# Optimization experiments

Measured on AMD Instinct MI355X. Metric: run time of the kernel, lower is better.

Reference implementation:

```python
import jax, jax.numpy as jnp
import numpy as np

N_ATOMS = 200000
MAX_DEG = 6
DEG_COUNTS = [2000, 40000, 60000, 58000, 38000, 1500, 500]  # atoms of degree 0..6, sorted by degree
_OFF = np.concatenate([[0], np.cumsum(DEG_COUNTS)])
BATCH = 1024
N_TASKS = 12
NAF = 75
BN_SCALE = np.float32(1.0 / np.sqrt(1.0 + 1e-5))  # eval-mode BN, running stats (0, 1)


def _split(x):
    # static degree slicing (atoms sorted by degree)
    return [x[_OFF[d]:_OFF[d + 1]] for d in range(MAX_DEG + 1)]


def graph_conv(x, adjs, W, b):
    # W: [2*MAX_DEG+1, in, out]; per degree d>=1 weights (2(d-1): neighbors, 2d-1: self), last: degree-0 self
    sp = _split(x)
    outs = [None] * (MAX_DEG + 1)
    for d in range(1, MAX_DEG + 1):
        summed = x[adjs[d - 1]].sum(axis=1)  # [n_d, in] sum over d neighbors
        o = summed @ W[2 * (d - 1)] + b[2 * (d - 1)]
        o = o + sp[d] @ W[2 * d - 1] + b[2 * d - 1]
        outs[d] = o
    outs[0] = sp[0] @ W[2 * MAX_DEG] + b[2 * MAX_DEG]
    return jax.nn.relu(jnp.concatenate(outs, axis=0))


def graph_pool(x, adjs):
    # max over {self} U neighbors, per degree
    sp = _split(x)
    outs = [sp[0]]
    for d in range(1, MAX_DEG + 1):
        neigh = x[adjs[d - 1]]  # [n_d, d, nf]
        outs.append(jnp.concatenate([sp[d][:, None, :], neigh], axis=1).max(axis=1))
    return jnp.concatenate(outs, axis=0)


def bn(x, gamma, beta):
    return x * (gamma * BN_SCALE) + beta


def _forward(atom_features, conv0_W, conv0_b, conv1_W, conv1_b,
             bn0_gamma, bn0_beta, bn1_gamma, bn1_beta, bn2_gamma, bn2_beta,
             bn3_gamma, bn3_beta, dense0_W, dense0_b, dense1_W, dense1_b,
             reg_W, reg_b, unc_W, unc_b, membership, adjs, n_samples):
    x = graph_conv(atom_features, adjs, conv0_W, conv0_b)
    x = bn(x, bn0_gamma, bn0_beta)
    x = graph_pool(x, adjs)
    x = graph_conv(x, adjs, conv1_W, conv1_b)
    x = bn(x, bn1_gamma, bn1_beta)
    x = graph_pool(x, adjs)
    x = bn(jax.nn.relu(x @ dense0_W + dense0_b), bn2_gamma, bn2_beta)
    x = bn(jax.nn.relu(x @ dense1_W + dense1_b), bn3_gamma, bn3_beta)
    fp = jnp.tanh(jax.ops.segment_sum(x, membership, num_segments=BATCH))  # GraphGather
    out = (fp @ reg_W + reg_b)[:n_samples]
    log_var = (fp @ unc_W + unc_b)[:n_samples]
    var = jnp.exp(log_var)
    return (out, var, out, log_var, fp)


def setup_inputs():
    key = jax.random.key(0)
    ks = jax.random.split(key, 32)
    inp = {}
    inp['atom_features'] = jax.random.normal(ks[0], (N_ATOMS, NAF), jnp.float32)
    inp['degree_slice'] = jnp.stack([jnp.asarray(_OFF[:-1], jnp.int32), jnp.asarray(DEG_COUNTS, jnp.int32)], axis=1)
    inp['membership'] = jax.random.randint(ks[1], (N_ATOMS,), 0, BATCH, jnp.int32)
    inp['n_samples'] = BATCH
    for d in range(1, MAX_DEG + 1):
        inp['deg_adj_%d' % d] = jax.random.randint(ks[1 + d], (DEG_COUNTS[d], d), 0, N_ATOMS, jnp.int32)
    def w(k, shape):
        return jax.random.normal(k, shape, jnp.float32) * 0.05
    nW = 2 * MAX_DEG + 1
    inp['conv0_W'] = w(ks[8], (nW, NAF, 128)); inp['conv0_b'] = w(ks[9], (nW, 128))
    inp['conv1_W'] = w(ks[10], (nW, 128, 128)); inp['conv1_b'] = w(ks[11], (nW, 128))
    inp['bn0_gamma'] = 1.0 + w(ks[12], (128,)); inp['bn0_beta'] = w(ks[13], (128,))
    inp['bn1_gamma'] = 1.0 + w(ks[14], (128,)); inp['bn1_beta'] = w(ks[15], (128,))
    inp['bn2_gamma'] = 1.0 + w(ks[16], (64,)); inp['bn2_beta'] = w(ks[17], (64,))
    inp['bn3_gamma'] = 1.0 + w(ks[18], (64,)); inp['bn3_beta'] = w(ks[19], (64,))
    inp['dense0_W'] = w(ks[20], (128, 64)); inp['dense0_b'] = w(ks[21], (64,))
    inp['dense1_W'] = w(ks[22], (64, 64)); inp['dense1_b'] = w(ks[23], (64,))
    inp['reg_W'] = w(ks[24], (64, N_TASKS)); inp['reg_b'] = w(ks[25], (N_TASKS,))
    inp['unc_W'] = w(ks[26], (64, N_TASKS)); inp['unc_b'] = w(ks[27], (N_TASKS,))
    return inp


def reference(atom_features, conv0_W, conv0_b, conv1_W, conv1_b,
              bn0_gamma, bn0_beta, bn1_gamma, bn1_beta, bn2_gamma, bn2_beta,
              bn3_gamma, bn3_beta, dense0_W, dense0_b, dense1_W, dense1_b,
              reg_W, reg_b, unc_W, unc_b,
              degree_slice, membership, n_samples,
              deg_adj_1, deg_adj_2, deg_adj_3, deg_adj_4, deg_adj_5, deg_adj_6):
    adjs = [deg_adj_1, deg_adj_2, deg_adj_3, deg_adj_4, deg_adj_5, deg_adj_6]
    return _forward(atom_features, conv0_W, conv0_b, conv1_W, conv1_b,
                    bn0_gamma, bn0_beta, bn1_gamma, bn1_beta, bn2_gamma, bn2_beta,
                    bn3_gamma, bn3_beta, dense0_W, dense0_b, dense1_W, dense1_b,
                    reg_W, reg_b, unc_W, unc_b, membership, adjs, n_samples)
```

## Files before the change

### kernel.cpp

```cpp
#include <hip/hip_runtime.h>
#include <math.h>

constexpr int OFFS[8] = {0, 2000, 42000, 102000, 160000, 198000, 199500, 200000};
constexpr int CNT[7]  = {2000, 40000, 60000, 58000, 38000, 1500, 500};
constexpr int C_OFF[8] = {0, 32, 657, 1595, 2502, 3096, 3120, 3128};
constexpr int P_OFF[8] = {0, 250, 5250, 12750, 20000, 24750, 24938, 25001};
#define BN_SCALE_C 0.9999950000374997f

struct Adjs { const int* a[6]; };

typedef __attribute__((ext_vector_type(8))) short bf16x8;
typedef __attribute__((ext_vector_type(4))) float f32x4;

__device__ __forceinline__ void split1(float x, ushort& h, ushort& l) {
    const unsigned u = __float_as_uint(x);
    h = (ushort)(u >> 16);
    const float r = x - __uint_as_float(u & 0xffff0000u);
    l = (ushort)(__float_as_uint(r) >> 16);
}

__global__ __launch_bounds__(256)
void w1_convert_kernel(const float* __restrict__ W, ushort* __restrict__ hi,
                       ushort* __restrict__ lo) {
    const int t = blockIdx.x * 256 + threadIdx.x;
    if (t >= 13 * 8 * 4 * 64 * 8) return;
    const int i = t & 7, l = (t >> 3) & 63, ks = (t >> 9) & 3,
              g = (t >> 11) & 7, s = t >> 14;
    const int col = g * 16 + (l & 15);
    const int k = ks * 32 + (l >> 4) * 8 + i;
    ushort h, lw;
    split1(W[(size_t)(s * 128 + k) * 128 + col], h, lw);
    hi[t] = h; lo[t] = lw;
}

__global__ __launch_bounds__(256)
void w0_convert_kernel(const float* __restrict__ W, ushort* __restrict__ hi,
                       ushort* __restrict__ lo) {
    const int t = blockIdx.x * 256 + threadIdx.x;
    if (t >= 7 * 8 * 5 * 64 * 8) return;
    const int i = t & 7;
    const int r = t >> 3;
    const int l = r & 63;
    const int r2 = r >> 6;
    const int ks = r2 % 5;
    const int r3 = r2 / 5;
    const int g = r3 & 7, d = r3 >> 3;
    const int col = g * 16 + (l & 15);
    const int k = ks * 32 + (l >> 4) * 8 + i;
    float v = 0.f;
    if (d == 0) {
        if (k < 75) v = W[(size_t)(12 * 75 + k) * 128 + col];
    } else {
        if (k < 75)       v = W[(size_t)((2 * d - 2) * 75 + k) * 128 + col];
        else if (k < 150) v = W[(size_t)((2 * d - 1) * 75 + (k - 75)) * 128 + col];
    }
    ushort h, lw;
    split1(v, h, lw);
    hi[t] = h; lo[t] = lw;
}

template<int KSTEPS, int SROW>
__device__ __forceinline__ void mfma_gemm(const ushort* sa_hi, const ushort* sa_lo,
                                          const ushort* wp_hi, const ushort* wp_lo,
                                          f32x4 acc[8], int l, int w)
{
    const int lr = l & 15, lq = l >> 4;
    const size_t lb = (size_t)l * 8;
    #pragma unroll
    for (int ks = 0; ks < KSTEPS; ++ks) {
        const int kb = ks * 32 + lq * 8;
        const bf16x8 ah = *(const bf16x8*)(sa_hi + (size_t)(w * 16 + lr) * SROW + kb);
        const bf16x8 al = *(const bf16x8*)(sa_lo + (size_t)(w * 16 + lr) * SROW + kb);
        bf16x8 bh0 = *(const bf16x8*)(wp_hi + (size_t)(0 * KSTEPS + ks) * 512 + lb);
        bf16x8 bl0 = *(const bf16x8*)(wp_lo + (size_t)(0 * KSTEPS + ks) * 512 + lb);
        bf16x8 bh1 = *(const bf16x8*)(wp_hi + (size_t)(1 * KSTEPS + ks) * 512 + lb);
        bf16x8 bl1 = *(const bf16x8*)(wp_lo + (size_t)(1 * KSTEPS + ks) * 512 + lb);
        #pragma unroll
        for (int g = 0; g < 8; ++g) {
            bf16x8 bh2 = bh0, bl2 = bl0;
            if (g < 6) {
                bh2 = *(const bf16x8*)(wp_hi + (size_t)((g + 2) * KSTEPS + ks) * 512 + lb);
                bl2 = *(const bf16x8*)(wp_lo + (size_t)((g + 2) * KSTEPS + ks) * 512 + lb);
            }
            acc[g] = __builtin_amdgcn_mfma_f32_16x16x32_bf16(ah, bh0, acc[g], 0, 0, 0);
            acc[g] = __builtin_amdgcn_mfma_f32_16x16x32_bf16(al, bh0, acc[g], 0, 0, 0);
            acc[g] = __builtin_amdgcn_mfma_f32_16x16x32_bf16(ah, bl0, acc[g], 0, 0, 0);
            bh0 = bh1; bl0 = bl1; bh1 = bh2; bl1 = bl2;
        }
    }
}

__device__ __forceinline__ void mfma_epilogue(f32x4 acc[8], float* fs,
                                              const float* s_eb, float* out,
                                              int a0, int nat, int tid)
{
    const int l = tid & 63, w = tid >> 6, lr = l & 15, lq = l >> 4;
    __syncthreads();
    #pragma unroll
    for (int g = 0; g < 8; ++g)
        #pragma unroll
        for (int r = 0; r < 4; ++r)
            fs[(size_t)(w * 16 + lq * 4 + r) * 132 + g * 16 + lr] = acc[g][r];
    __syncthreads();
    #pragma unroll
    for (int p = 0; p < 8; ++p) {
        const int row = p * 8 + (tid >> 5);
        if (row < nat) {
            const int c = (tid & 31) * 4;
            const float4 v  = *(const float4*)&fs[(size_t)row * 132 + c];
            const float4 bb = *(const float4*)&s_eb[c];
            const float4 gs = *(const float4*)&s_eb[128 + c];
            const float4 be = *(const float4*)&s_eb[256 + c];
            float4 o;
            o.x = fmaxf(v.x + bb.x, 0.f) * gs.x + be.x;
            o.y = fmaxf(v.y + bb.y, 0.f) * gs.y + be.y;
            o.z = fmaxf(v.z + bb.z, 0.f) * gs.z + be.z;
            o.w = fmaxf(v.w + bb.w, 0.f) * gs.w + be.w;
            *(float4*)(out + (size_t)(a0 + row) * 128 + c) = o;
        }
    }
}

template<int D>
__device__ __forceinline__ void conv0_body(int tile, const float* __restrict__ x,
    const ushort* __restrict__ wp_hi, const ushort* __restrict__ wp_lo,
    const float* __restrict__ b, const float* __restrict__ gamma,
    const float* __restrict__ beta, const int* __restrict__ adjp,
    float* __restrict__ out, ushort* s_ahi, ushort* s_alo, int* s_adj,
    float* s_eb, int tid)
{
    constexpr int SROW = 168;
    const int a0 = OFFS[D] + tile * 64;
    const int nat = min(64, OFFS[D + 1] - a0);

    if (tid < 128) {
        float bb;
        if constexpr (D > 0)
            bb = b[(2 * D - 2) * 128 + tid] + b[(2 * D - 1) * 128 + tid];
        else
            bb = b[12 * 128 + tid];
        s_eb[tid] = bb;
        s_eb[128 + tid] = gamma[tid] * BN_SCALE_C;
        s_eb[256 + tid] = beta[tid];
    }
    if constexpr (D > 0) {
        for (int e = tid; e < 64 * D; e += 256) {
            const int al = e / D;
            if (al < nat)
                s_adj[e] = adjp[(size_t)(a0 - OFFS[D] + al) * D + (e - al * D)];
        }
        __syncthreads();
    }
    if constexpr (D == 0) {
        for (int e = tid; e < 64 * 85; e += 256) {
            const int al = e / 85, k = 75 + e - (e / 85) * 85;
            s_ahi[al * SROW + k] = 0; s_alo[al * SROW + k] = 0;
        }
    } else {
        for (int e = tid; e < 64 * 10; e += 256) {
            const int al = e / 10, k = 150 + e - (e / 10) * 10;
            s_ahi[al * SROW + k] = 0; s_alo[al * SROW + k] = 0;
        }
    }
    #pragma unroll 4
    for (int p = 0; p < 19; ++p) {
        const int e = p * 256 + tid;
        if (e < 4800) {
            const int al = e / 75;
            const int kk = e - al * 75;
            if (al < nat) {
                const float self = x[(size_t)(a0 + al) * 75 + kk];
                ushort h, l;
                if constexpr (D > 0) {
                    float sum = 0.f;
                    #pragma unroll
                    for (int i = 0; i < D; ++i)
                        sum += x[(size_t)s_adj[al * D + i] * 75 + kk];
                    split1(sum, h, l);
                    s_ahi[al * SROW + kk] = h; s_alo[al * SROW + kk] = l;
                    split1(self, h, l);
                    s_ahi[al * SROW + 75 + kk] = h; s_alo[al * SROW + 75 + kk] = l;
                } else {
                    split1(self, h, l);
                    s_ahi[al * SROW + kk] = h; s_alo[al * SROW + kk] = l;
                }
            }
        }
    }
    __syncthreads();

    const int l = tid & 63, w = tid >> 6;
    f32x4 acc[8];
    #pragma unroll
    for (int g = 0; g < 8; ++g) acc[g] = (f32x4){0.f, 0.f, 0.f, 0.f};
    mfma_gemm<5, SROW>(s_ahi, s_alo, wp_hi + (size_t)D * 20480,
                       wp_lo + (size_t)D * 20480, acc, l, w);
    mfma_epilogue(acc, (float*)s_ahi, s_eb, out, a0, nat, tid);
}

__global__ __launch_bounds__(256, 3)
void conv0_merged(const float* __restrict__ x, const ushort* __restrict__ wp_hi,
                  const ushort* __restrict__ wp_lo, const float* __restrict__ b,
                  const float* __restrict__ gamma, const float* __restrict__ beta,
                  Adjs adj, float* __restrict__ out)
{
    __shared__ ushort s_a[2][64 * 168];
    __shared__ int s_adj[64 * 6];
    __shared__ float s_eb[384];
    const int blk = blockIdx.x, tid = threadIdx.x;
    #define C0(D) conv0_body<D>(blk - C_OFF[D], x, wp_hi, wp_lo, b, gamma, beta, \
        (D > 0) ? adj.a[D - 1] : nullptr, out, s_a[0], s_a[1], s_adj, s_eb, tid)
    if      (blk < C_OFF[1]) C0(0);
    else if (blk < C_OFF[2]) C0(1);
    else if (blk < C_OFF[3]) C0(2);
    else if (blk < C_OFF[4]) C0(3);
    else if (blk < C_OFF[5]) C0(4);
    else if (blk < C_OFF[6]) C0(5);
    else                     C0(6);
    #undef C0
}

template<int D, bool PHASE0>
__device__ __forceinline__ void conv1_stage(const float* __restrict__ x,
    ushort* s_ahi, ushort* s_alo, const int* s_adj, int a0, int nat, int tid)
{
    constexpr int SROW = 136;
    #pragma unroll 2
    for (int p = 0; p < 8; ++p) {
        const int e = p * 256 + tid;
        const int al = e >> 5, c = e & 31;
        if (al < nat) {
            float4 v;
            if (PHASE0 && D > 0) {
                v = make_float4(0.f, 0.f, 0.f, 0.f);
                #pragma unroll
                for (int i = 0; i < D; ++i) {
                    const float4 t = *((const float4*)(x + (size_t)s_adj[al * D + i] * 128) + c);
                    v.x += t.x; v.y += t.y; v.z += t.z; v.w += t.w;
                }
            } else {
                v = *((const float4*)(x + (size_t)(a0 + al) * 128) + c);
            }
            ushort4 h, lo;
            split1(v.x, h.x, lo.x); split1(v.y, h.y, lo.y);
            split1(v.z, h.z, lo.z); split1(v.w, h.w, lo.w);
            *(ushort4*)&s_ahi[al * SROW + c * 4] = h;
            *(ushort4*)&s_alo[al * SROW + c * 4] = lo;
        }
    }
}

template<int D>
__device__ __forceinline__ void conv1_body(int tile, const float* __restrict__ x,
    const ushort* __restrict__ wp_hi, const ushort* __restrict__ wp_lo,
    const float* __restrict__ b, const float* __restrict__ gamma,
    const float* __restrict__ beta, const int* __restrict__ adjp,
    float* __restrict__ out, ushort* s_ahi, ushort* s_alo, int* s_adj,
    float* s_eb, int tid)
{
    constexpr int SROW = 136;
    const int a0 = OFFS[D] + tile * 64;
    const int nat = min(64, OFFS[D + 1] - a0);

    if (tid < 128) {
        float bb;
        if constexpr (D > 0)
            bb = b[(2 * D - 2) * 128 + tid] + b[(2 * D - 1) * 128 + tid];
        else
            bb = b[12 * 128 + tid];
        s_eb[tid] = bb;
        s_eb[128 + tid] = gamma[tid] * BN_SCALE_C;
        s_eb[256 + tid] = beta[tid];
    }
    if constexpr (D > 0) {
        for (int e = tid; e < 64 * D; e += 256) {
            const int al = e / D;
            if (al < nat)
                s_adj[e] = adjp[(size_t)(a0 - OFFS[D] + al) * D + (e - al * D)];
        }
        __syncthreads();
    }

    const int l = tid & 63, w = tid >> 6;
    f32x4 acc[8];
    #pragma unroll
    for (int g = 0; g < 8; ++g) acc[g] = (f32x4){0.f, 0.f, 0.f, 0.f};

    conv1_stage<D, true>(x, s_ahi, s_alo, s_adj, a0, nat, tid);
    __syncthreads();
    {
        const size_t wb = (size_t)((D == 0) ? 12 : (2 * D - 2)) * 16384;
        mfma_gemm<4, SROW>(s_ahi, s_alo, wp_hi + wb, wp_lo + wb, acc, l, w);
    }
    if constexpr (D > 0) {
        __syncthreads();
        conv1_stage<D, false>(x, s_ahi, s_alo, s_adj, a0, nat, tid);
        __syncthreads();
        const size_t wb = (size_t)(2 * D - 1) * 16384;
        mfma_gemm<4, SROW>(s_ahi, s_alo, wp_hi + wb, wp_lo + wb, acc, l, w);
    }
    mfma_epilogue(acc, (float*)s_ahi, s_eb, out, a0, nat, tid);
}

__global__ __launch_bounds__(256, 4)
void conv1_merged(const float* __restrict__ x, const ushort* __restrict__ wp_hi,
                  const ushort* __restrict__ wp_lo, const float* __restrict__ b,
                  const float* __restrict__ gamma, const float* __restrict__ beta,
                  Adjs adj, float* __restrict__ out)
{
    __shared__ ushort s_a[2][64 * 136];
    __shared__ int s_adj[64 * 6];
    __shared__ float s_eb[384];
    const int blk = blockIdx.x, tid = threadIdx.x;
    #define C1(D) conv1_body<D>(blk - C_OFF[D], x, wp_hi, wp_lo, b, gamma, beta, \
        (D > 0) ? adj.a[D - 1] : nullptr, out, s_a[0], s_a[1], s_adj, s_eb, tid)
    if      (blk < C_OFF[1]) C1(0);
    else if (blk < C_OFF[2]) C1(1);
    else if (blk < C_OFF[3]) C1(2);
    else if (blk < C_OFF[4]) C1(3);
    else if (blk < C_OFF[5]) C1(4);
    else if (blk < C_OFF[6]) C1(5);
    else                     C1(6);
    #undef C1
}

template<int D>
__device__ __forceinline__ void pool_body(int tile, const float* __restrict__ x,
    const int* __restrict__ adjp, float* __restrict__ out, int tid)
{
    const int tx = tid & 31;
    const int ai = tile * 8 + (tid >> 5);
    if (ai >= CNT[D]) return;
    const int a = OFFS[D] + ai;
    float4 v = *((const float4*)(x + (size_t)a * 128) + tx);
    if constexpr (D > 0) {
        #pragma unroll
        for (int i = 0; i < D; ++i) {
            const int n = adjp[(size_t)ai * D + i];
            const float4 t = *((const float4*)(x + (size_t)n * 128) + tx);
            v.x = fmaxf(v.x, t.x); v.y = fmaxf(v.y, t.y);
            v.z = fmaxf(v.z, t.z); v.w = fmaxf(v.w, t.w);
        }
    }
    *((float4*)(out + (size_t)a * 128) + tx) = v;
}

__global__ __launch_bounds__(256)
void pool_merged(const float* __restrict__ x, Adjs adj, float* __restrict__ out)
{
    const int blk = blockIdx.x, tid = threadIdx.x;
    #define PB(D) pool_body<D>(blk - P_OFF[D], x, (D > 0) ? adj.a[D - 1] : nullptr, out, tid)
    if      (blk < P_OFF[1]) PB(0);
    else if (blk < P_OFF[2]) PB(1);
    else if (blk < P_OFF[3]) PB(2);
    else if (blk < P_OFF[4]) PB(3);
    else if (blk < P_OFF[5]) PB(4);
    else if (blk < P_OFF[6]) PB(5);
    else                     PB(6);
    #undef PB
}

__global__ __launch_bounds__(256, 2)
void dense0_pool_kernel(const float* __restrict__ x, const float* __restrict__ W,
                        const float* __restrict__ b, const float* __restrict__ gamma,
                        const float* __restrict__ beta, Adjs adj,
                        float* __restrict__ out)
{
    __shared__ float s_a[64][132];
    __shared__ float s_w[128][64];
    const int tid = threadIdx.x;
    const int a0 = blockIdx.x * 64;
    {
        const int tx4 = tid & 31, ag = tid >> 5;
        #pragma unroll
        for (int ap = 0; ap < 8; ++ap) {
            const int al = ap * 8 + ag;
            const int a = a0 + al;
            int d, base = 0;
            if      (a < 2000)   { d = 0; }
            else if (a < 42000)  { d = 1; base = 2000; }
            else if (a < 102000) { d = 2; base = 42000; }
            else if (a < 160000) { d = 3; base = 102000; }
            else if (a < 198000) { d = 4; base = 160000; }
            else if (a < 199500) { d = 5; base = 198000; }
            else                 { d = 6; base = 199500; }
            float4 v = *((const float4*)(x + (size_t)a * 128) + tx4);
            if (d > 0) {
                const int* arow = adj.a[d - 1] + (size_t)(a - base) * d;
                for (int i = 0; i < d; ++i) {
                    const float4 t = *((const float4*)(x + (size_t)arow[i] * 128) + tx4);
                    v.x = fmaxf(v.x, t.x); v.y = fmaxf(v.y, t.y);
                    v.z = fmaxf(v.z, t.z); v.w = fmaxf(v.w, t.w);
                }
            }
            *(float4*)&s_a[al][tx4 * 4] = v;
        }
    }
    #pragma unroll
    for (int p = 0; p < 8; ++p) {
        const int f = p * 256 + tid;
        const int r = f >> 4, c = (f & 15) * 4;
        *(float4*)&s_w[r][c] = *(const float4*)(W + r * 64 + c);
    }
    __syncthreads();

    const int tx = tid & 15, ty = tid >> 4;
    float acc[4][4];
    #pragma unroll
    for (int i = 0; i < 4; ++i)
        #pragma unroll
        for (int j = 0; j < 4; ++j) acc[i][j] = 0.f;

    #pragma unroll 8
    for (int k = 0; k < 128; ++k) {
        const float4 w = *(float4*)&s_w[k][tx * 4];
        #pragma unroll
        for (int i = 0; i < 4; ++i) {
            const float av = s_a[ty * 4 + i][k];
            acc[i][0] = fmaf(av, w.x, acc[i][0]);
            acc[i][1] = fmaf(av, w.y, acc[i][1]);
            acc[i][2] = fmaf(av, w.z, acc[i][2]);
            acc[i][3] = fmaf(av, w.w, acc[i][3]);
        }
    }
    const int j = tx * 4;
    float bb[4], gs[4], be[4];
    #pragma unroll
    for (int c = 0; c < 4; ++c) {
        bb[c] = b[j + c]; gs[c] = gamma[j + c] * BN_SCALE_C; be[c] = beta[j + c];
    }
    #pragma unroll
    for (int i = 0; i < 4; ++i) {
        const int al = ty * 4 + i;
        float4 o;
        o.x = fmaxf(acc[i][0] + bb[0], 0.f) * gs[0] + be[0];
        o.y = fmaxf(acc[i][1] + bb[1], 0.f) * gs[1] + be[1];
        o.z = fmaxf(acc[i][2] + bb[2], 0.f) * gs[2] + be[2];
        o.w = fmaxf(acc[i][3] + bb[3], 0.f) * gs[3] + be[3];
        *(float4*)(out + (size_t)(a0 + al) * 64 + j) = o;
    }
}

__global__ void zero_counts_kernel(int* __restrict__ counts) {
    counts[blockIdx.x * 256 + threadIdx.x] = 0;
}

__global__ __launch_bounds__(256)
void hist_kernel(const int* __restrict__ mem, int* __restrict__ counts) {
    const int a = blockIdx.x * 256 + threadIdx.x;
    if (a < 200000) atomicAdd(&counts[mem[a]], 1);
}

__global__ __launch_bounds__(1024)
void scan_kernel(const int* __restrict__ counts, int* __restrict__ starts,
                 int* __restrict__ cursor) {
    __shared__ int s[1024];
    const int tid = threadIdx.x;
    s[tid] = counts[tid];
    __syncthreads();
    #pragma unroll
    for (int off = 1; off < 1024; off <<= 1) {
        const int v = (tid >= off) ? s[tid - off] : 0;
        __syncthreads();
        s[tid] += v;
        __syncthreads();
    }
    const int st = (tid == 0) ? 0 : s[tid - 1];
    starts[tid] = st;
    cursor[tid] = st;
    if (tid == 1023) starts[1024] = s[1023];
}

__global__ __launch_bounds__(256)
void scatter_kernel(const int* __restrict__ mem, int* __restrict__ cursor,
                    int* __restrict__ idx) {
    const int a = blockIdx.x * 256 + threadIdx.x;
    if (a < 200000) {
        const int p = atomicAdd(&cursor[mem[a]], 1);
        idx[p] = a;
    }
}

__global__ __launch_bounds__(256, 4)
void seg_dense1_kernel(const float* __restrict__ y0, const float* __restrict__ W,
                       const float* __restrict__ b, const float* __restrict__ gamma,
                       const float* __restrict__ beta, const int* __restrict__ idx,
                       const int* __restrict__ starts, float* __restrict__ accum)
{
    __shared__ float s_a[64][68];
    __shared__ float s_w[64][64];
    __shared__ float s_red[16][64];
    const int tid = threadIdx.x;
    const int seg = blockIdx.x;
    const int s0 = starts[seg];
    const int cnt = starts[seg + 1] - s0;

    #pragma unroll
    for (int p = 0; p < 4; ++p) {
        const int f = p * 256 + tid;
        const int r = f >> 4, c = (f & 15) * 4;
        *(float4*)&s_w[r][c] = *(const float4*)(W + r * 64 + c);
    }

    const int tx = tid & 15, ty = tid >> 4;
    const int j = tx * 4;
    float bb[4], gs[4], be[4];
    #pragma unroll
    for (int c = 0; c < 4; ++c) {
        bb[c] = b[j + c]; gs[c] = gamma[j + c] * BN_SCALE_C; be[c] = beta[j + c];
    }
    float facc[4] = {0.f, 0.f, 0.f, 0.f};

    for (int t0 = 0; t0 < cnt; t0 += 64) {
        const int nt = min(64, cnt - t0);
        __syncthreads();
        #pragma unroll
        for (int p = 0; p < 4; ++p) {
            const int e = p * 256 + tid;
            const int al = e >> 4, c = e & 15;
            if (al < nt) {
                const int a = idx[s0 + t0 + al];
                *(float4*)&s_a[al][c * 4] = *((const float4*)(y0 + (size_t)a * 64) + c);
            }
        }
        __syncthreads();
        float acc[4][4];
        #pragma unroll
        for (int i = 0; i < 4; ++i)
            #pragma unroll
            for (int c = 0; c < 4; ++c) acc[i][c] = 0.f;
        #pragma unroll 8
        for (int k = 0; k < 64; ++k) {
            const float4 w = *(float4*)&s_w[k][tx * 4];
            #pragma unroll
            for (int i = 0; i < 4; ++i) {
                const float av = s_a[ty * 4 + i][k];
                acc[i][0] = fmaf(av, w.x, acc[i][0]);
                acc[i][1] = fmaf(av, w.y, acc[i][1]);
                acc[i][2] = fmaf(av, w.z, acc[i][2]);
                acc[i][3] = fmaf(av, w.w, acc[i][3]);
            }
        }
        #pragma unroll
        for (int i = 0; i < 4; ++i) {
            if (ty * 4 + i < nt) {
                #pragma unroll
                for (int c = 0; c < 4; ++c)
                    facc[c] += fmaxf(acc[i][c] + bb[c], 0.f) * gs[c] + be[c];
            }
        }
    }
    __syncthreads();
    #pragma unroll
    for (int c = 0; c < 4; ++c) s_red[ty][j + c] = facc[c];
    __syncthreads();
    if (tid < 64) {
        float s = 0.f;
        #pragma unroll
        for (int q = 0; q < 16; ++q) s += s_red[q][tid];
        accum[(size_t)seg * 64 + tid] = s;
    }
}

__global__ __launch_bounds__(256)
void final_kernel(const float* __restrict__ accum,
                  const float* __restrict__ regW, const float* __restrict__ regb,
                  const float* __restrict__ uncW, const float* __restrict__ uncb,
                  float* __restrict__ out)
{
    __shared__ float s_f[256];
    const int tid = threadIdx.x;
    const int rl = tid >> 6;
    const int c = tid & 63;
    const int r = blockIdx.x * 4 + rl;
    const float f = tanhf(accum[(size_t)r * 64 + c]);
    out[49152 + (size_t)r * 64 + c] = f;
    s_f[tid] = f;
    __syncthreads();
    if (c < 24) {
        const bool isreg = (c < 12);
        const int t = isreg ? c : c - 12;
        const float* Wm = isreg ? regW : uncW;
        float a = isreg ? regb[t] : uncb[t];
        #pragma unroll 8
        for (int k = 0; k < 64; ++k)
            a = fmaf(s_f[rl * 64 + k], Wm[k * 12 + t], a);
        if (isreg) {
            out[(size_t)r * 12 + t] = a;
            out[24576 + (size_t)r * 12 + t] = a;
        } else {
            out[36864 + (size_t)r * 12 + t] = a;
            out[12288 + (size_t)r * 12 + t] = expf(a);
        }
    }
}

extern "C" void kernel_launch(void* const* d_in, const int* in_sizes, int n_in,
                              void* d_out, int out_size, void* d_ws, size_t ws_size,
                              hipStream_t stream)
{
    const float* atom_features = (const float*)d_in[0];
    const int*   membership    = (const int*)d_in[2];
    Adjs adj;
    for (int d = 1; d <= 6; ++d) adj.a[d - 1] = (const int*)d_in[3 + d];
    const float* conv0_W = (const float*)d_in[10];
    const float* conv0_b = (const float*)d_in[11];
    const float* conv1_W = (const float*)d_in[12];
    const float* conv1_b = (const float*)d_in[13];
    const float* bn0_g = (const float*)d_in[14];
    const float* bn0_b = (const float*)d_in[15];
    const float* bn1_g = (const float*)d_in[16];
    const float* bn1_b = (const float*)d_in[17];
    const float* bn2_g = (const float*)d_in[18];
    const float* bn2_b = (const float*)d_in[19];
    const float* bn3_g = (const float*)d_in[20];
    const float* bn3_b = (const float*)d_in[21];
    const float* dense0_W = (const float*)d_in[22];
    const float* dense0_b = (const float*)d_in[23];
    const float* dense1_W = (const float*)d_in[24];
    const float* dense1_b = (const float*)d_in[25];
    const float* reg_W = (const float*)d_in[26];
    const float* reg_b = (const float*)d_in[27];
    const float* unc_W = (const float*)d_in[28];
    const float* unc_b = (const float*)d_in[29];

    float* ws    = (float*)d_ws;
    float* buf0  = ws;
    float* buf1  = ws + 25600000;
    float* accum = ws + 51200000;
    int*   idx     = (int*)(ws + 51265536);
    int*   counts  = (int*)(ws + 51465536);
    int*   starts  = (int*)(ws + 51466560);
    int*   cursor  = (int*)(ws + 51467585);
    ushort* wp1_hi = (ushort*)(ws + 51468800);
    ushort* wp1_lo = (ushort*)(ws + 51575296);
    ushort* wp0_hi = (ushort*)(ws + 51681792);
    ushort* wp0_lo = (ushort*)(ws + 51753472);

    w1_convert_kernel<<<832, 256, 0, stream>>>(conv1_W, wp1_hi, wp1_lo);
    w0_convert_kernel<<<560, 256, 0, stream>>>(conv0_W, wp0_hi, wp0_lo);
    zero_counts_kernel<<<4, 256, 0, stream>>>(counts);
    hist_kernel<<<782, 256, 0, stream>>>(membership, counts);
    scan_kernel<<<1, 1024, 0, stream>>>(counts, starts, cursor);
    scatter_kernel<<<782, 256, 0, stream>>>(membership, cursor, idx);

    conv0_merged<<<3128, 256, 0, stream>>>(atom_features, wp0_hi, wp0_lo, conv0_b,
                                           bn0_g, bn0_b, adj, buf0);
    pool_merged<<<25001, 256, 0, stream>>>(buf0, adj, buf1);
    conv1_merged<<<3128, 256, 0, stream>>>(buf1, wp1_hi, wp1_lo, conv1_b,
                                           bn1_g, bn1_b, adj, buf0);
    dense0_pool_kernel<<<3125, 256, 0, stream>>>(buf0, dense0_W, dense0_b,
                                                 bn2_g, bn2_b, adj, buf1);
    seg_dense1_kernel<<<1024, 256, 0, stream>>>(buf1, dense1_W, dense1_b,
                                                bn3_g, bn3_b, idx, starts, accum);
    final_kernel<<<256, 256, 0, stream>>>(accum, reg_W, reg_b, unc_W, unc_b, (float*)d_out);
}
```

Before: 586.9 us.

## Split fused pool+dense0 kernel by degree and read weights from global

Rewrites the fused second-pool and dense0 kernel so each block handles 64 atoms of a single degree, with the degree known at compile time. Neighbor indices are staged in shared memory, which removes the per-atom degree branching and variable-length loops. The 32KB shared weight tile is dropped in favour of float4 reads of W from global or cache, and A is read as float4 from shared memory; the smaller shared footprint allows a higher occupancy bound (4 blocks). The risks are extra global or L1 weight traffic per FMA and partially filled tiles at degree boundaries.

```diff
diff --git a/kernel.cpp b/kernel.cpp
--- a/kernel.cpp
+++ b/kernel.cpp
@@ -360,85 +360,119 @@
     #undef PB
 }
 
-__global__ __launch_bounds__(256, 2)
-void dense0_pool_kernel(const float* __restrict__ x, const float* __restrict__ W,
+template<int D>
+__device__ __forceinline__ void d0_body(int tile, const float* __restrict__ x,
+    const float* __restrict__ W, const float* __restrict__ b,
+    const float* __restrict__ gamma, const float* __restrict__ beta,
+    const int* __restrict__ adjp, float* __restrict__ out,
+    float* s_a , int* s_adj, int tid)
+{
+    const int a0 = OFFS[D] + tile * 64;
+    const int nat = min(64, OFFS[D + 1] - a0);
+
+    if constexpr (D > 0) {
+        for (int e = tid; e < 64 * D; e += 256) {
+            const int al = e / D;
+            if (al < nat)
+                s_adj[e] = adjp[(size_t)(a0 - OFFS[D] + al) * D + (e - al * D)];
+        }
+        __syncthreads();
+    }
+    {
+        const int tx4 = tid & 31, ag = tid >> 5;
+        #pragma unroll
+        for (int ap = 0; ap < 8; ++ap) {
+            const int al = ap * 8 + ag;
+            if (al < nat) {
+                float4 v = *((const float4*)(x + (size_t)(a0 + al) * 128) + tx4);
+                if constexpr (D > 0) {
+                    #pragma unroll
+                    for (int i = 0; i < D; ++i) {
+                        const float4 t =
+                            *((const float4*)(x + (size_t)s_adj[al * D + i] * 128) + tx4);
+                        v.x = fmaxf(v.x, t.x); v.y = fmaxf(v.y, t.y);
+                        v.z = fmaxf(v.z, t.z); v.w = fmaxf(v.w, t.w);
+                    }
+                }
+                *(float4*)&s_a[al * 132 + tx4 * 4] = v;
+            }
+        }
+    }
+    __syncthreads();
+
+    const int tx = tid & 15, ty = tid >> 4;
+    float acc[4][4];
+    #pragma unroll
+    for (int i = 0; i < 4; ++i)
+        #pragma unroll
+        for (int j = 0; j < 4; ++j) acc[i][j] = 0.f;
+
+    #pragma unroll 4
+    for (int k4 = 0; k4 < 32; ++k4) {
+        float4 wk[4];
+        #pragma unroll
+        for (int kk = 0; kk < 4; ++kk)
+            wk[kk] = *(const float4*)(W + (size_t)(k4 * 4 + kk) * 64 + tx * 4);
+        #pragma unroll
+        for (int i = 0; i < 4; ++i) {
+            const float4 av = *(const float4*)&s_a[(ty * 4 + i) * 132 + k4 * 4];
+            acc[i][0] = fmaf(av.x, wk[0].x, acc[i][0]);
+            acc[i][1] = fmaf(av.x, wk[0].y, acc[i][1]);
+            acc[i][2] = fmaf(av.x, wk[0].z, acc[i][2]);
+            acc[i][3] = fmaf(av.x, wk[0].w, acc[i][3]);
+            acc[i][0] = fmaf(av.y, wk[1].x, acc[i][0]);
+            acc[i][1] = fmaf(av.y, wk[1].y, acc[i][1]);
+            acc[i][2] = fmaf(av.y, wk[1].z, acc[i][2]);
+            acc[i][3] = fmaf(av.y, wk[1].w, acc[i][3]);
+            acc[i][0] = fmaf(av.z, wk[2].x, acc[i][0]);
+            acc[i][1] = fmaf(av.z, wk[2].y, acc[i][1]);
+            acc[i][2] = fmaf(av.z, wk[2].z, acc[i][2]);
+            acc[i][3] = fmaf(av.z, wk[2].w, acc[i][3]);
+            acc[i][0] = fmaf(av.w, wk[3].x, acc[i][0]);
+            acc[i][1] = fmaf(av.w, wk[3].y, acc[i][1]);
+            acc[i][2] = fmaf(av.w, wk[3].z, acc[i][2]);
+            acc[i][3] = fmaf(av.w, wk[3].w, acc[i][3]);
+        }
+    }
+    const int j = tx * 4;
+    float bb[4], gs[4], be[4];
+    #pragma unroll
+    for (int c = 0; c < 4; ++c) {
+        bb[c] = b[j + c]; gs[c] = gamma[j + c] * BN_SCALE_C; be[c] = beta[j + c];
+    }
+    #pragma unroll
+    for (int i = 0; i < 4; ++i) {
+        const int al = ty * 4 + i;
+        if (al < nat) {
+            float4 o;
+            o.x = fmaxf(acc[i][0] + bb[0], 0.f) * gs[0] + be[0];
+            o.y = fmaxf(acc[i][1] + bb[1], 0.f) * gs[1] + be[1];
+            o.z = fmaxf(acc[i][2] + bb[2], 0.f) * gs[2] + be[2];
+            o.w = fmaxf(acc[i][3] + bb[3], 0.f) * gs[3] + be[3];
+            *(float4*)(out + (size_t)(a0 + al) * 64 + j) = o;
+        }
+    }
+}
+
+__global__ __launch_bounds__(256, 4)
+void dense0_pool_merged(const float* __restrict__ x, const float* __restrict__ W,
                         const float* __restrict__ b, const float* __restrict__ gamma,
                         const float* __restrict__ beta, Adjs adj,
                         float* __restrict__ out)
 {
-    __shared__ float s_a[64][132];
-    __shared__ float s_w[128][64];
-    const int tid = threadIdx.x;
-    const int a0 = blockIdx.x * 64;
-    {
-        const int tx4 = tid & 31, ag = tid >> 5;
-        #pragma unroll
-        for (int ap = 0; ap < 8; ++ap) {
-            const int al = ap * 8 + ag;
-            const int a = a0 + al;
-            int d, base = 0;
-            if      (a < 2000)   { d = 0; }
-            else if (a < 42000)  { d = 1; base = 2000; }
-            else if (a < 102000) { d = 2; base = 42000; }
-            else if (a < 160000) { d = 3; base = 102000; }
-            else if (a < 198000) { d = 4; base = 160000; }
-            else if (a < 199500) { d = 5; base = 198000; }
-            else                 { d = 6; base = 199500; }
-            float4 v = *((const float4*)(x + (size_t)a * 128) + tx4);
-            if (d > 0) {
-                const int* arow = adj.a[d - 1] + (size_t)(a - base) * d;
-                for (int i = 0; i < d; ++i) {
-                    const float4 t = *((const float4*)(x + (size_t)arow[i] * 128) + tx4);
-                    v.x = fmaxf(v.x, t.x); v.y = fmaxf(v.y, t.y);
-                    v.z = fmaxf(v.z, t.z); v.w = fmaxf(v.w, t.w);
-                }
-            }
-            *(float4*)&s_a[al][tx4 * 4] = v;
-        }
-    }
-    #pragma unroll
-    for (int p = 0; p < 8; ++p) {
-        const int f = p * 256 + tid;
-        const int r = f >> 4, c = (f & 15) * 4;
-        *(float4*)&s_w[r][c] = *(const float4*)(W + r * 64 + c);
-    }
-    __syncthreads();
-
-    const int tx = tid & 15, ty = tid >> 4;
-    float acc[4][4];
-    #pragma unroll
-    for (int i = 0; i < 4; ++i)
-        #pragma unroll
-        for (int j = 0; j < 4; ++j) acc[i][j] = 0.f;
-
-    #pragma unroll 8
-    for (int k = 0; k < 128; ++k) {
-        const float4 w = *(float4*)&s_w[k][tx * 4];
-        #pragma unroll
-        for (int i = 0; i < 4; ++i) {
-            const float av = s_a[ty * 4 + i][k];
-            acc[i][0] = fmaf(av, w.x, acc[i][0]);
-            acc[i][1] = fmaf(av, w.y, acc[i][1]);
-            acc[i][2] = fmaf(av, w.z, acc[i][2]);
-            acc[i][3] = fmaf(av, w.w, acc[i][3]);
-        }
-    }
-    const int j = tx * 4;
-    float bb[4], gs[4], be[4];
-    #pragma unroll
-    for (int c = 0; c < 4; ++c) {
-        bb[c] = b[j + c]; gs[c] = gamma[j + c] * BN_SCALE_C; be[c] = beta[j + c];
-    }
-    #pragma unroll
-    for (int i = 0; i < 4; ++i) {
-        const int al = ty * 4 + i;
-        float4 o;
-        o.x = fmaxf(acc[i][0] + bb[0], 0.f) * gs[0] + be[0];
-        o.y = fmaxf(acc[i][1] + bb[1], 0.f) * gs[1] + be[1];
-        o.z = fmaxf(acc[i][2] + bb[2], 0.f) * gs[2] + be[2];
-        o.w = fmaxf(acc[i][3] + bb[3], 0.f) * gs[3] + be[3];
-        *(float4*)(out + (size_t)(a0 + al) * 64 + j) = o;
-    }
+    __shared__ float s_a[64 * 132];
+    __shared__ int s_adj[64 * 6];
+    const int blk = blockIdx.x, tid = threadIdx.x;
+    #define D0(D) d0_body<D>(blk - C_OFF[D], x, W, b, gamma, beta, \
+        (D > 0) ? adj.a[D - 1] : nullptr, out, s_a, s_adj, tid)
+    if      (blk < C_OFF[1]) D0(0);
+    else if (blk < C_OFF[2]) D0(1);
+    else if (blk < C_OFF[3]) D0(2);
+    else if (blk < C_OFF[4]) D0(3);
+    else if (blk < C_OFF[5]) D0(4);
+    else if (blk < C_OFF[6]) D0(5);
+    else                     D0(6);
+    #undef D0
 }
 
 __global__ void zero_counts_kernel(int* __restrict__ counts) {
@@ -649,7 +683,7 @@
     pool_merged<<<25001, 256, 0, stream>>>(buf0, adj, buf1);
     conv1_merged<<<3128, 256, 0, stream>>>(buf1, wp1_hi, wp1_lo, conv1_b,
                                            bn1_g, bn1_b, adj, buf0);
-    dense0_pool_kernel<<<3125, 256, 0, stream>>>(buf0, dense0_W, dense0_b,
+    dense0_pool_merged<<<3128, 256, 0, stream>>>(buf0, dense0_W, dense0_b,
                                                  bn2_g, bn2_b, adj, buf1);
     seg_dense1_kernel<<<1024, 256, 0, stream>>>(buf1, dense1_W, dense1_b,
                                                 bn3_g, bn3_b, idx, starts, accum);
```

After: 533.7 us. -9.1%, faster.
